# Kernel optimization log

Hardware: AMD Instinct MI355X
Metric: run time of the kernel (lower is better)

The kernel has to match this reference:

```python
import jax, jax.numpy as jnp
import numpy as np

B, NQ, NV, DIM, H, F = 32, 197, 1568, 768, 12, 8


def setup_inputs() -> dict:
    key = jax.random.key(0)
    ks = jax.random.split(key, 5)
    return {
        "x": jax.random.normal(ks[0], (B, NV, DIM), jnp.float32),
        "question": jax.random.normal(ks[1], (B, NQ, DIM), jnp.float32),
        "Wq": jax.random.normal(ks[2], (DIM, DIM), jnp.float32) * 0.02,
        "Wkv": jax.random.normal(ks[3], (DIM, 2 * DIM), jnp.float32) * 0.02,
        "Wproj": jax.random.normal(ks[4], (DIM, DIM), jnp.float32) * 0.02,
        "bproj": jnp.zeros((DIM,), jnp.float32),
        "f": F,
    }


def _heads(t, h):
    # 'b n (h d) -> (b h) n d'
    b, n, dim = t.shape
    d = dim // h
    return t.reshape(b, n, h, d).transpose(0, 2, 1, 3).reshape(b * h, n, d)


def reference(x, question, Wq, Wkv, Wproj, bproj, f):
    b, nv, dim = x.shape
    h = H
    d = dim // h
    scale = d ** -0.5

    q = _heads(question @ Wq, h) * scale          # (bh, nq, d), pre-scaled as in source
    kv = x @ Wkv
    k = _heads(kv[..., :dim], h)                  # (bh, nv, d)
    v = _heads(kv[..., dim:], h)                  # (bh, nv, d)

    cls_q, q_ = q[:, :1], q[:, 1:]                # cls token vs patch queries

    # cls token attends over ALL video tokens
    cls_sim = jnp.einsum('bid,bjd->bij', cls_q, k)
    cls_out = jnp.einsum('bij,bjd->bid', jax.nn.softmax(cls_sim, axis=-1), v)

    # patch queries attend per-frame: k,v 'b (f n) d -> (b f) n d', q_ repeat_interleave(f)
    n = nv // f
    kf = k.reshape(b * h, f, n, d)
    vf = v.reshape(b * h, f, n, d)
    sim = jnp.einsum('bqd,bfkd->bfqk', q_, kf)    # broadcast == repeat_interleave over frames
    out = jnp.einsum('bfqk,bfkd->bfqd', jax.nn.softmax(sim, axis=-1), vf)
    out = out.reshape(b * h, f * (q.shape[1] - 1), d)  # '(b f) n d -> b (f n) d'

    out = jnp.concatenate([cls_out, out], axis=1)  # (bh, 1 + f*(nq-1), d)
    n_out = out.shape[1]
    # '(b h) n d -> b n (h d)'
    out = out.reshape(b, h, n_out, d).transpose(0, 2, 1, 3).reshape(b, n_out, dim)
    return out @ Wproj + bproj
```

## Files before the change

### kernel.cpp

```cpp
#include <hip/hip_runtime.h>

typedef __bf16 bf16;
typedef __bf16 bf16x8 __attribute__((ext_vector_type(8)));
typedef __bf16 bf16x4 __attribute__((ext_vector_type(4)));
typedef __bf16 bf16x2 __attribute__((ext_vector_type(2)));
typedef float f32x4 __attribute__((ext_vector_type(4)));
typedef float f32x16 __attribute__((ext_vector_type(16)));
typedef unsigned int u32x4 __attribute__((ext_vector_type(4)));

#define MFMA16(a, b, c) __builtin_amdgcn_mfma_f32_16x16x32_bf16(a, b, c, 0, 0, 0)
#define MFMA32(a, b, c) __builtin_amdgcn_mfma_f32_32x32x16_bf16(a, b, c, 0, 0, 0)

__device__ __forceinline__ void gload_lds16(const bf16* g, bf16* l) {
  __builtin_amdgcn_global_load_lds(
      (const __attribute__((address_space(1))) void*)g,
      (__attribute__((address_space(3))) void*)l, 16, 0, 0);
}

__device__ __forceinline__ unsigned pk2(float a, float b) {
  bf16x2 t;
  t[0] = (bf16)a;
  t[1] = (bf16)b;
  return __builtin_bit_cast(unsigned, t);
}

__device__ __forceinline__ void wg_barrier() {
  __builtin_amdgcn_sched_barrier(0);
  asm volatile("s_barrier" ::: "memory");
  __builtin_amdgcn_sched_barrier(0);
}

__global__ __launch_bounds__(256) void f2b_k(const float* __restrict__ src,
                                             bf16* __restrict__ dst,
                                             long long n) {
  long long i = ((long long)blockIdx.x * 256 + threadIdx.x) * 8;
  if (i >= n) return;
  const float4 a = *(const float4*)(src + i);
  const float4 b = *(const float4*)(src + i + 4);
  bf16x8 v;
  v[0] = (bf16)a.x; v[1] = (bf16)a.y; v[2] = (bf16)a.z; v[3] = (bf16)a.w;
  v[4] = (bf16)b.x; v[5] = (bf16)b.y; v[6] = (bf16)b.z; v[7] = (bf16)b.w;
  *(bf16x8*)(dst + i) = v;
}

__global__ __launch_bounds__(256) void wconv_k(const float* __restrict__ W,
                                               bf16* __restrict__ Wt,
                                               int K, int N) {
  long long idx = (long long)blockIdx.x * 256 + threadIdx.x;
  if (idx >= (long long)K * N) return;
  int k = (int)(idx % K);
  int n = (int)(idx / K);
  Wt[idx] = (bf16)W[(long long)k * N + n];
}

__global__ __launch_bounds__(256) void pad0_k(bf16* __restrict__ Vt) {
  long long idx = (long long)blockIdx.x * 256 + threadIdx.x;
  const long long total = 3072LL * 64 * 7;
  if (idx >= total) return;
  int c = (int)(idx % 7);
  long long t = idx / 7;
  int d = (int)(t % 64);
  long long f = t / 64;
  bf16x4 z = {};
  *(bf16x4*)&Vt[(f * 64 + d) * 224 + 196 + c * 4] = z;
}

template <int MODE>
__global__ __launch_bounds__(256) void gemm_k(const bf16* __restrict__ A,
                                              const bf16* __restrict__ Bt,
                                              void* __restrict__ Cptr,
                                              const float* __restrict__ bias,
                                              int M, int N, int K) {
  __shared__ bf16 As[128 * 64];
  __shared__ bf16 Bs[128 * 64];
  const int tid = threadIdx.x;
  const int lane = tid & 63, w = tid >> 6;
  const int wm = w & 1, wn = w >> 1;
  const int col = lane & 15, quad = lane >> 4;
  const int m0 = blockIdx.x * 128, n0 = blockIdx.y * 128;

  const int rsub = lane >> 3;
  const int segg = (lane & 7) ^ rsub;
  const bf16* Ag0 = A + (long long)(m0 + w * 32 + rsub) * K + segg * 8;
  const bf16* Bg0 = Bt + (long long)(n0 + w * 32 + rsub) * K + segg * 8;
  bf16* Al0 = As + (w * 32) * 64;
  bf16* Bl0 = Bs + (w * 32) * 64;

  f32x4 acc[4][4] = {};
  const int sA = col & 7;

  for (int k0 = 0; k0 < K; k0 += 64) {
    __syncthreads();
#pragma unroll
    for (int j = 0; j < 4; ++j)
      gload_lds16(Ag0 + (long long)j * 8 * K + k0, Al0 + j * 8 * 64);
#pragma unroll
    for (int j = 0; j < 4; ++j)
      gload_lds16(Bg0 + (long long)j * 8 * K + k0, Bl0 + j * 8 * 64);
    __syncthreads();

#pragma unroll
    for (int kk2 = 0; kk2 < 2; ++kk2) {
      const int s = kk2 * 4 + quad;
      const int slot = (s ^ sA) * 8;
      bf16x8 af[4], bfr[4];
#pragma unroll
      for (int mt = 0; mt < 4; ++mt)
        af[mt] = *(const bf16x8*)&As[(wm * 64 + mt * 16 + col) * 64 + slot];
#pragma unroll
      for (int nt = 0; nt < 4; ++nt)
        bfr[nt] = *(const bf16x8*)&Bs[(wn * 64 + nt * 16 + col) * 64 + slot];
#pragma unroll
      for (int mt = 0; mt < 4; ++mt) {
#pragma unroll
        for (int nt = 0; nt < 4; ++nt)
          acc[mt][nt] = MFMA16(af[mt], bfr[nt], acc[mt][nt]);
      }
    }
  }

#pragma unroll
  for (int mt = 0; mt < 4; ++mt) {
#pragma unroll
    for (int nt = 0; nt < 4; ++nt) {
      const int gn = n0 + wn * 64 + nt * 16 + col;
#pragma unroll
      for (int r = 0; r < 4; ++r) {
        const int gm = m0 + wm * 64 + mt * 16 + quad * 4 + r;
        if (gm >= M) continue;
        const float v = acc[mt][nt][r];
        ((bf16*)Cptr)[(long long)gm * N + gn] = (bf16)(v * 0.125f);
      }
    }
  }
}

template <int MODE>
__global__ __launch_bounds__(512) void gemm256_k(
    const bf16* __restrict__ A, const bf16* __restrict__ Bt,
    void* __restrict__ Cptr, bf16* __restrict__ C2,
    const float* __restrict__ bias, int M, int N, int K,
    int NB, int qq, int rq) {
  __shared__ bf16 As[2][256 * 64];
  __shared__ bf16 Bs[2][256 * 64];
  const int tid = threadIdx.x;
  const int lane = tid & 63, w = tid >> 6;
  const int wm = w & 1, wn = w >> 1;
  const int col = lane & 15, quad = lane >> 4;

  const int bid = blockIdx.x;
  const int xcd = bid & 7, ii = bid >> 3;
  const int wg = (xcd < rq ? xcd * (qq + 1) : rq * (qq + 1) + (xcd - rq) * qq) + ii;
  const int mb = wg / NB, nb = wg - mb * NB;
  const int m0 = mb * 256, n0 = nb * 256;

  const int rsub = lane >> 3;
  const int segg = (lane & 7) ^ rsub;
  const bf16* Ag0 = A + (long long)(m0 + w * 32 + rsub) * K + segg * 8;
  const bf16* Bg0 = Bt + (long long)(n0 + w * 32 + rsub) * K + segg * 8;
  const int lbase = (w * 32) * 64;

  f32x4 acc[8][4] = {};
  const int sA = col & 7;

#pragma unroll
  for (int j = 0; j < 4; ++j) {
    gload_lds16(Ag0 + (long long)j * 8 * K, &As[0][lbase + j * 8 * 64]);
    gload_lds16(Bg0 + (long long)j * 8 * K, &Bs[0][lbase + j * 8 * 64]);
  }

  const int NT = K >> 6;
  for (int t = 0; t < NT; ++t) {
    const int cur = t & 1;
    if (t + 1 < NT) {
      const long long koff = (long long)(t + 1) * 64;
#pragma unroll
      for (int j = 0; j < 4; ++j) {
        gload_lds16(Ag0 + (long long)j * 8 * K + koff,
                    &As[cur ^ 1][lbase + j * 8 * 64]);
        gload_lds16(Bg0 + (long long)j * 8 * K + koff,
                    &Bs[cur ^ 1][lbase + j * 8 * 64]);
      }
      asm volatile("s_waitcnt vmcnt(8)");
    } else {
      asm volatile("s_waitcnt vmcnt(0)");
    }
    wg_barrier();

#pragma unroll
    for (int kk2 = 0; kk2 < 2; ++kk2) {
      const int slot = ((kk2 * 4 + quad) ^ sA) << 3;
      bf16x8 af[8], bfv[4];
#pragma unroll
      for (int mt = 0; mt < 8; ++mt)
        af[mt] = *(const bf16x8*)&As[cur][(wm * 128 + mt * 16 + col) * 64 + slot];
#pragma unroll
      for (int nt = 0; nt < 4; ++nt)
        bfv[nt] = *(const bf16x8*)&Bs[cur][(wn * 64 + nt * 16 + col) * 64 + slot];
      __builtin_amdgcn_s_setprio(1);
#pragma unroll
      for (int mt = 0; mt < 8; ++mt) {
#pragma unroll
        for (int nt = 0; nt < 4; ++nt)
          acc[mt][nt] = MFMA16(af[mt], bfv[nt], acc[mt][nt]);
      }
      __builtin_amdgcn_s_setprio(0);
    }
    wg_barrier();
  }

  if (MODE == 1) {
    bf16* Kbp = (bf16*)Cptr;
#pragma unroll
    for (int mt = 0; mt < 8; ++mt) {
      const int gm0 = m0 + wm * 128 + mt * 16 + quad * 4;
      if (gm0 >= M) continue;
      const int bb = gm0 / 1568;
      const int j0 = gm0 - bb * 1568;
      const int fr = j0 / 196;
      const int kk0 = j0 - fr * 196;
#pragma unroll
      for (int nt = 0; nt < 4; ++nt) {
        const int gn = n0 + wn * 64 + nt * 16 + col;
        if (gn < 768) {
          const int hh = gn >> 6, dd = gn & 63;
          bf16* kp = Kbp + ((long long)(bb * 12 + hh) * 1568 + j0) * 64 + dd;
#pragma unroll
          for (int r = 0; r < 4; ++r) kp[r * 64] = (bf16)acc[mt][nt][r];
        } else {
          const int g2 = gn - 768;
          const int hh = g2 >> 6, dd = g2 & 63;
          bf16x4 pv;
          pv[0] = (bf16)acc[mt][nt][0];
          pv[1] = (bf16)acc[mt][nt][1];
          pv[2] = (bf16)acc[mt][nt][2];
          pv[3] = (bf16)acc[mt][nt][3];
          *(bf16x4*)&C2[(((long long)(bb * 12 + hh) * 8 + fr) * 64 + dd) * 224 +
                        kk0] = pv;
        }
      }
    }
  } else {
#pragma unroll
    for (int mt = 0; mt < 8; ++mt) {
#pragma unroll
      for (int nt = 0; nt < 4; ++nt) {
        const int gn = n0 + wn * 64 + nt * 16 + col;
        const float bv = bias[gn];
#pragma unroll
        for (int r = 0; r < 4; ++r) {
          const int gm = m0 + wm * 128 + mt * 16 + quad * 4 + r;
          if (gm < M)
            ((float*)Cptr)[(long long)gm * N + gn] = acc[mt][nt][r] + bv;
        }
      }
    }
  }
}

__global__ __launch_bounds__(256) void attn_k(const bf16* __restrict__ qs,
                                              const bf16* __restrict__ Kb,
                                              const bf16* __restrict__ Vt,
                                              bf16* __restrict__ Ob) {
  __shared__ bf16 Ks[224 * 64];
  const int bh = blockIdx.x, fr = blockIdx.y;
  const int b = bh / 12, h = bh % 12;
  const int tid = threadIdx.x, lane = tid & 63, w = tid >> 6;
  const int col = lane & 31, half = lane >> 5;
  const bf16* Qb = qs + (long long)b * 197 * 768 + h * 64;
  const bf16* Kbase = Kb + ((long long)bh * 1568 + fr * 196) * 64;
  const bf16* Vbase = Vt + (long long)(bh * 8 + fr) * 64 * 224;

  {
    const int rsub = lane >> 3;
    const int segg = (lane & 7) ^ rsub;
    const bf16* g0 = Kbase + (long long)(w * 56 + rsub) * 64 + segg * 8;
    bf16* l0 = Ks + (w * 56) * 64;
#pragma unroll
    for (int j = 0; j < 7; ++j)
      gload_lds16(g0 + (long long)j * 8 * 64, l0 + j * 8 * 64);
  }
  __syncthreads();

  for (int mt = w; mt < 7; mt += 4) {
    const int qq = mt * 32 + col;
    const int tok = (qq < 196) ? qq + 1 : 196;
    const bf16* qp = Qb + (long long)tok * 768 + half * 8;
    bf16x8 qf[4];
#pragma unroll
    for (int t = 0; t < 4; ++t) qf[t] = *(const bf16x8*)(qp + 16 * t);

    f32x16 o0 = {}, o1 = {};
    float m = -1e30f, l = 0.f;

#pragma unroll 2
    for (int nt = 0; nt < 7; ++nt) {
      bf16x8 vf[4];
#pragma unroll
      for (int wdw = 0; wdw < 2; ++wdw)
#pragma unroll
        for (int dt = 0; dt < 2; ++dt)
          vf[wdw * 2 + dt] = *(const bf16x8*)(Vbase +
              (long long)(dt * 32 + col) * 224 + nt * 32 + wdw * 16 + half * 8);

      f32x16 s = {};
#pragma unroll
      for (int t = 0; t < 4; ++t) {
        const int row = nt * 32 + col;
        const int sgm = 2 * t + half;
        const bf16x8 kf =
            *(const bf16x8*)&Ks[row * 64 + ((sgm ^ (row & 7)) << 3)];
        s = MFMA32(kf, qf[t], s);
      }
      if (nt == 6) {
#pragma unroll
        for (int r = 0; r < 16; ++r) {
          if (r >= 4) s[r] = -1e30f;
          else if (half) s[r] = -1e30f;
        }
      }

      float tm = s[0];
#pragma unroll
      for (int r = 1; r < 16; ++r) tm = fmaxf(tm, s[r]);
      tm = fmaxf(tm, __shfl_xor(tm, 32, 64));

      if (__any(tm > m + 8.f)) {
        const float mn = fmaxf(m, tm);
        const float sc = __expf(m - mn);
        l *= sc;
#pragma unroll
        for (int r = 0; r < 16; ++r) {
          const float scr = __shfl(sc, (r & 3) + 8 * (r >> 2) + 4 * half, 64);
          o0[r] *= scr;
          o1[r] *= scr;
        }
        m = mn;
      }

      float ls = 0.f;
#pragma unroll
      for (int r = 0; r < 16; ++r) {
        s[r] = __expf(s[r] - m);
        ls += s[r];
      }
      l += ls;
      unsigned pk[8];
#pragma unroll
      for (int i = 0; i < 8; ++i) pk[i] = pk2(s[2 * i], s[2 * i + 1]);

#pragma unroll
      for (int wdw = 0; wdw < 2; ++wdw) {
        const unsigned xa = half ? pk[4 * wdw + 0] : pk[4 * wdw + 2];
        const unsigned xb = half ? pk[4 * wdw + 1] : pk[4 * wdw + 3];
        const unsigned ya = __shfl_xor(xa, 32, 64);
        const unsigned yb = __shfl_xor(xb, 32, 64);
        const unsigned oa = half ? pk[4 * wdw + 2] : pk[4 * wdw + 0];
        const unsigned ob = half ? pk[4 * wdw + 3] : pk[4 * wdw + 1];
        u32x4 wv;
        wv[0] = half ? ya : oa;
        wv[1] = half ? yb : ob;
        wv[2] = half ? oa : ya;
        wv[3] = half ? ob : yb;
        const bf16x8 pa = __builtin_bit_cast(bf16x8, wv);
        o0 = MFMA32(pa, vf[wdw * 2 + 0], o0);
        o1 = MFMA32(pa, vf[wdw * 2 + 1], o1);
      }
    }

    const float lt = l + __shfl_xor(l, 32, 64);
    const float inv = 1.f / lt;
#pragma unroll
    for (int r = 0; r < 16; ++r) {
      const int qr = (r & 3) + 8 * (r >> 2) + 4 * half;
      const float invr = __shfl(inv, qr, 64);
      const int q2 = mt * 32 + qr;
      if (q2 < 196) {
        const int token = 1 + fr * 196 + q2;
        bf16* op = Ob + ((long long)b * 1569 + token) * 768 + h * 64 + col;
        op[0] = (bf16)(o0[r] * invr);
        op[32] = (bf16)(o1[r] * invr);
      }
    }
  }
}

__global__ __launch_bounds__(256) void cls_k(const bf16* __restrict__ qs,
                                             const bf16* __restrict__ Kb,
                                             const bf16* __restrict__ Vt,
                                             bf16* __restrict__ Ob) {
  __shared__ float qsm[64];
  __shared__ float ssm[1568];
  __shared__ float red[256];
  __shared__ float osm[4][64];
  const int bh = blockIdx.x;
  const int b = bh / 12, h = bh % 12;
  const int tid = threadIdx.x;
  if (tid < 64) qsm[tid] = (float)qs[(long long)b * 197 * 768 + h * 64 + tid];
  __syncthreads();

  float lmax = -1e30f;
  for (int j = tid; j < 1568; j += 256) {
    const bf16* kp = Kb + ((long long)bh * 1568 + j) * 64;
    float s = 0.f;
#pragma unroll
    for (int seg = 0; seg < 8; ++seg) {
      const bf16x8 kv = *(const bf16x8*)(kp + seg * 8);
#pragma unroll
      for (int i = 0; i < 8; ++i) s += qsm[seg * 8 + i] * (float)kv[i];
    }
    ssm[j] = s;
    lmax = fmaxf(lmax, s);
  }
  red[tid] = lmax;
  __syncthreads();
  for (int sft = 128; sft > 0; sft >>= 1) {
    if (tid < sft) red[tid] = fmaxf(red[tid], red[tid + sft]);
    __syncthreads();
  }
  const float mx = red[0];
  __syncthreads();

  float lsum = 0.f;
  for (int j = tid; j < 1568; j += 256) {
    const float p = __expf(ssm[j] - mx);
    ssm[j] = p;
    lsum += p;
  }
  red[tid] = lsum;
  __syncthreads();
  for (int sft = 128; sft > 0; sft >>= 1) {
    if (tid < sft) red[tid] += red[tid + sft];
    __syncthreads();
  }
  const float inv = 1.f / red[0];
  __syncthreads();

  const int d = tid & 63, c = tid >> 6;
  float acc = 0.f;
  for (int fr = c * 2; fr < c * 2 + 2; ++fr) {
    const bf16* vp = Vt + ((long long)(bh * 8 + fr) * 64 + d) * 224;
    const float* pp = &ssm[fr * 196];
    for (int k = 0; k < 196; ++k) acc += pp[k] * (float)vp[k];
  }
  osm[c][d] = acc;
  __syncthreads();
  if (tid < 64) {
    const float o = (osm[0][tid] + osm[1][tid] + osm[2][tid] + osm[3][tid]) * inv;
    Ob[(long long)b * 1569 * 768 + h * 64 + tid] = (bf16)o;
  }
}

extern "C" void kernel_launch(void* const* d_in, const int* in_sizes, int n_in,
                              void* d_out, int out_size, void* d_ws, size_t ws_size,
                              hipStream_t stream) {
  const float* x        = (const float*)d_in[0];
  const float* question = (const float*)d_in[1];
  const float* Wq       = (const float*)d_in[2];
  const float* Wkv      = (const float*)d_in[3];
  const float* Wproj    = (const float*)d_in[4];
  const float* bproj    = (const float*)d_in[5];
  float* out = (float*)d_out;

  char* wsb = (char*)d_ws;
  const long long SZ_WQT  = 768LL * 768 * 2;
  const long long SZ_WKVT = 1536LL * 768 * 2;
  const long long SZ_WPT  = 768LL * 768 * 2;
  const long long SZ_QNB  = 32LL * 197 * 768 * 2;
  const long long SZ_Q    = 32LL * 197 * 768 * 2;
  const long long SZ_XO   = 50208LL * 768 * 2;
  const long long SZ_K    = 384LL * 1568 * 64 * 2;

  long long off = 0;
  bf16* Wqt  = (bf16*)(wsb + off); off += SZ_WQT;
  bf16* Wkvt = (bf16*)(wsb + off); off += SZ_WKVT;
  bf16* Wpt  = (bf16*)(wsb + off); off += SZ_WPT;
  bf16* qnb  = (bf16*)(wsb + off); off += SZ_QNB;
  bf16* qsb  = (bf16*)(wsb + off); off += SZ_Q;
  bf16* xb   = (bf16*)(wsb + off);
  bf16* Ob   = xb;
  off += SZ_XO;
  bf16* Kb   = (bf16*)(wsb + off); off += SZ_K;
  bf16* Vt   = (bf16*)(wsb + off);

  const long long nx = 32LL * 1568 * 768;
  const long long nq = 32LL * 197 * 768;
  f2b_k<<<(int)((nx / 8 + 255) / 256), 256, 0, stream>>>(x, xb, nx);
  f2b_k<<<(int)((nq / 8 + 255) / 256), 256, 0, stream>>>(question, qnb, nq);

  wconv_k<<<(768 * 768) / 256, 256, 0, stream>>>(Wq, Wqt, 768, 768);
  wconv_k<<<(768 * 1536) / 256, 256, 0, stream>>>(Wkv, Wkvt, 768, 1536);
  wconv_k<<<(768 * 768) / 256, 256, 0, stream>>>(Wproj, Wpt, 768, 768);
  pad0_k<<<(3072 * 64 * 7) / 256, 256, 0, stream>>>(Vt);

  gemm_k<0><<<dim3(50, 6), 256, 0, stream>>>(qnb, Wqt, qsb, nullptr,
                                             6304, 768, 768);
  gemm256_k<1><<<1176, 512, 0, stream>>>(xb, Wkvt, Kb, Vt, nullptr,
                                         50176, 1536, 768, 6, 147, 0);

  cls_k<<<384, 256, 0, stream>>>(qsb, Kb, Vt, Ob);
  attn_k<<<dim3(384, 8), 256, 0, stream>>>(qsb, Kb, Vt, Ob);

  gemm256_k<2><<<591, 512, 0, stream>>>(Ob, Wpt, out, nullptr, bproj,
                                        50208, 768, 768, 3, 73, 7);
}
```

Before: 823.6 us.

## Split GEMM K-step into four quadrant phases with staggered A/B prefetch

Restructures the GEMM main loop into four MFMA phases, one per 4x2 quadrant of the accumulator tile. LDS fragment reads are interleaved between the phases, and the A and B global-to-LDS prefetches are issued at different points. The aim is to overlap LDS reads and global loads with MFMA work in a ping-pong style schedule and to lower register pressure by holding fewer fragments at once. It adds more workgroup barriers per K-step and relies on sched_barrier, which could serialize execution if waves do not interleave as intended.

```diff
diff --git a/kernel.cpp b/kernel.cpp
--- a/kernel.cpp
+++ b/kernel.cpp
@@ -164,48 +164,113 @@
   const int sA = col & 7;
 
 #pragma unroll
-  for (int j = 0; j < 4; ++j) {
+  for (int j = 0; j < 4; ++j)
     gload_lds16(Ag0 + (long long)j * 8 * K, &As[0][lbase + j * 8 * 64]);
+#pragma unroll
+  for (int j = 0; j < 4; ++j)
     gload_lds16(Bg0 + (long long)j * 8 * K, &Bs[0][lbase + j * 8 * 64]);
-  }
 
   const int NT = K >> 6;
+  bf16x8 aA[4][2], bA[2][2], bB[2][2];
+
   for (int t = 0; t < NT; ++t) {
     const int cur = t & 1;
-    if (t + 1 < NT) {
-      const long long koff = (long long)(t + 1) * 64;
-#pragma unroll
-      for (int j = 0; j < 4; ++j) {
+    const bool pf = (t + 1 < NT);
+    const long long koff = (long long)(t + 1) * 64;
+
+    if (pf) {
+#pragma unroll
+      for (int j = 0; j < 4; ++j)
         gload_lds16(Ag0 + (long long)j * 8 * K + koff,
                     &As[cur ^ 1][lbase + j * 8 * 64]);
+      __builtin_amdgcn_sched_barrier(0);
+      asm volatile("s_waitcnt vmcnt(4)");
+      __builtin_amdgcn_sched_barrier(0);
+    } else {
+      __builtin_amdgcn_sched_barrier(0);
+      asm volatile("s_waitcnt vmcnt(0)");
+      __builtin_amdgcn_sched_barrier(0);
+    }
+    wg_barrier();
+#pragma unroll
+    for (int ks = 0; ks < 2; ++ks) {
+      const int slot = ((ks * 4 + quad) ^ sA) << 3;
+#pragma unroll
+      for (int mt = 0; mt < 4; ++mt)
+        aA[mt][ks] =
+            *(const bf16x8*)&As[cur][(wm * 128 + mt * 16 + col) * 64 + slot];
+#pragma unroll
+      for (int nt = 0; nt < 2; ++nt)
+        bA[nt][ks] =
+            *(const bf16x8*)&Bs[cur][(wn * 64 + nt * 16 + col) * 64 + slot];
+    }
+    __builtin_amdgcn_s_setprio(1);
+#pragma unroll
+    for (int ks = 0; ks < 2; ++ks)
+#pragma unroll
+      for (int mt = 0; mt < 4; ++mt)
+#pragma unroll
+        for (int nt = 0; nt < 2; ++nt)
+          acc[mt][nt] = MFMA16(aA[mt][ks], bA[nt][ks], acc[mt][nt]);
+    __builtin_amdgcn_s_setprio(0);
+    wg_barrier();
+
+#pragma unroll
+    for (int ks = 0; ks < 2; ++ks) {
+      const int slot = ((ks * 4 + quad) ^ sA) << 3;
+#pragma unroll
+      for (int nt = 0; nt < 2; ++nt)
+        bB[nt][ks] = *(const bf16x8*)&Bs[cur][(wn * 64 + (nt + 2) * 16 + col) *
+                                                  64 + slot];
+    }
+    if (pf) {
+#pragma unroll
+      for (int j = 0; j < 4; ++j)
         gload_lds16(Bg0 + (long long)j * 8 * K + koff,
                     &Bs[cur ^ 1][lbase + j * 8 * 64]);
-      }
-      asm volatile("s_waitcnt vmcnt(8)");
-    } else {
-      asm volatile("s_waitcnt vmcnt(0)");
-    }
-    wg_barrier();
-
-#pragma unroll
-    for (int kk2 = 0; kk2 < 2; ++kk2) {
-      const int slot = ((kk2 * 4 + quad) ^ sA) << 3;
-      bf16x8 af[8], bfv[4];
-#pragma unroll
-      for (int mt = 0; mt < 8; ++mt)
-        af[mt] = *(const bf16x8*)&As[cur][(wm * 128 + mt * 16 + col) * 64 + slot];
-#pragma unroll
-      for (int nt = 0; nt < 4; ++nt)
-        bfv[nt] = *(const bf16x8*)&Bs[cur][(wn * 64 + nt * 16 + col) * 64 + slot];
-      __builtin_amdgcn_s_setprio(1);
-#pragma unroll
-      for (int mt = 0; mt < 8; ++mt) {
-#pragma unroll
-        for (int nt = 0; nt < 4; ++nt)
-          acc[mt][nt] = MFMA16(af[mt], bfv[nt], acc[mt][nt]);
-      }
-      __builtin_amdgcn_s_setprio(0);
-    }
+    }
+    wg_barrier();
+    __builtin_amdgcn_s_setprio(1);
+#pragma unroll
+    for (int ks = 0; ks < 2; ++ks)
+#pragma unroll
+      for (int mt = 0; mt < 4; ++mt)
+#pragma unroll
+        for (int nt = 0; nt < 2; ++nt)
+          acc[mt][nt + 2] = MFMA16(aA[mt][ks], bB[nt][ks], acc[mt][nt + 2]);
+    __builtin_amdgcn_s_setprio(0);
+    wg_barrier();
+
+#pragma unroll
+    for (int ks = 0; ks < 2; ++ks) {
+      const int slot = ((ks * 4 + quad) ^ sA) << 3;
+#pragma unroll
+      for (int mt = 0; mt < 4; ++mt)
+        aA[mt][ks] = *(const bf16x8*)&As[cur][(wm * 128 + (mt + 4) * 16 + col) *
+                                                  64 + slot];
+    }
+    wg_barrier();
+    __builtin_amdgcn_s_setprio(1);
+#pragma unroll
+    for (int ks = 0; ks < 2; ++ks)
+#pragma unroll
+      for (int mt = 0; mt < 4; ++mt)
+#pragma unroll
+        for (int nt = 0; nt < 2; ++nt)
+          acc[mt + 4][nt + 2] =
+              MFMA16(aA[mt][ks], bB[nt][ks], acc[mt + 4][nt + 2]);
+    __builtin_amdgcn_s_setprio(0);
+    wg_barrier();
+
+    __builtin_amdgcn_s_setprio(1);
+#pragma unroll
+    for (int ks = 0; ks < 2; ++ks)
+#pragma unroll
+      for (int mt = 0; mt < 4; ++mt)
+#pragma unroll
+        for (int nt = 0; nt < 2; ++nt)
+          acc[mt + 4][nt] = MFMA16(aA[mt][ks], bA[nt][ks], acc[mt + 4][nt]);
+    __builtin_amdgcn_s_setprio(0);
     wg_barrier();
   }
 
```

Result: no change. 819.8 us (-0.5%).

## Make KV projection GEMM persistent with cross-tile prefetch of next job

Applied to the files above, without the earlier changes.

Replaces the 1176-block KV projection GEMM with a persistent kernel of 256 blocks. Each block loops over 4-5 output tiles, with tiles grouped by XCD (blockIdx & 7). The first K-slice of the next tile is prefetched while the last slice of the current one is computed. This removes launch and tail effects and hides the pipeline fill between tiles. The cost is a fixed schedule hardcoded to these shapes, plus the loss of the M-bound check in the epilogue.

```diff
diff --git a/kernel.cpp b/kernel.cpp
--- a/kernel.cpp
+++ b/kernel.cpp
@@ -209,12 +209,120 @@
     wg_barrier();
   }
 
-  if (MODE == 1) {
-    bf16* Kbp = (bf16*)Cptr;
+#pragma unroll
+  for (int mt = 0; mt < 8; ++mt) {
+#pragma unroll
+    for (int nt = 0; nt < 4; ++nt) {
+      const int gn = n0 + wn * 64 + nt * 16 + col;
+      const float bv = bias[gn];
+#pragma unroll
+      for (int r = 0; r < 4; ++r) {
+        const int gm = m0 + wm * 128 + mt * 16 + quad * 4 + r;
+        if (gm < M)
+          ((float*)Cptr)[(long long)gm * N + gn] = acc[mt][nt][r] + bv;
+      }
+    }
+  }
+}
+
+__global__ __launch_bounds__(512) void gemmp_k(const bf16* __restrict__ A,
+                                               const bf16* __restrict__ Bt,
+                                               bf16* __restrict__ Kb,
+                                               bf16* __restrict__ Vt) {
+  __shared__ bf16 As[2][256 * 64];
+  __shared__ bf16 Bs[2][256 * 64];
+  const int tid = threadIdx.x;
+  const int lane = tid & 63, w = tid >> 6;
+  const int wm = w & 1, wn = w >> 1;
+  const int col = lane & 15, quad = lane >> 4;
+
+  const int b = blockIdx.x;
+  const int xcd = b & 7, sub = b >> 3;
+  const int base = xcd * 147;
+  const int njobs = (sub <= 18) ? 5 : 4;
+
+  const int rsub = lane >> 3;
+  const int segg = (lane & 7) ^ rsub;
+  const int lbase = (w * 32) * 64;
+  const int sA = col & 7;
+
+  f32x4 acc[8][4] = {};
+
+  int jj = base + sub;
+  int mb = jj / 6;
+  int m0 = mb * 256, n0 = (jj - mb * 6) * 256;
+
+  {
+    const bf16* Ag = A + (long long)(m0 + w * 32 + rsub) * 768 + segg * 8;
+    const bf16* Bg = Bt + (long long)(n0 + w * 32 + rsub) * 768 + segg * 8;
+#pragma unroll
+    for (int j = 0; j < 4; ++j) {
+      gload_lds16(Ag + (long long)j * 8 * 768, &As[0][lbase + j * 8 * 64]);
+      gload_lds16(Bg + (long long)j * 8 * 768, &Bs[0][lbase + j * 8 * 64]);
+    }
+  }
+
+  int tglob = 0;
+  for (int g = 0; g < njobs; ++g) {
+    int m0n = 0, n0n = 0;
+    const bool hasNext = (g + 1 < njobs);
+    if (hasNext) {
+      const int j2 = base + sub + 32 * (g + 1);
+      const int mb2 = j2 / 6;
+      m0n = mb2 * 256;
+      n0n = (j2 - mb2 * 6) * 256;
+    }
+
+    for (int kt = 0; kt < 12; ++kt, ++tglob) {
+      const int cur = tglob & 1;
+      if (kt < 11 || hasNext) {
+        const int sm0 = (kt < 11) ? m0 : m0n;
+        const int sn0 = (kt < 11) ? n0 : n0n;
+        const int skt = (kt < 11) ? kt + 1 : 0;
+        const bf16* Ag =
+            A + (long long)(sm0 + w * 32 + rsub) * 768 + skt * 64 + segg * 8;
+        const bf16* Bg =
+            Bt + (long long)(sn0 + w * 32 + rsub) * 768 + skt * 64 + segg * 8;
+#pragma unroll
+        for (int j = 0; j < 4; ++j) {
+          gload_lds16(Ag + (long long)j * 8 * 768,
+                      &As[cur ^ 1][lbase + j * 8 * 64]);
+          gload_lds16(Bg + (long long)j * 8 * 768,
+                      &Bs[cur ^ 1][lbase + j * 8 * 64]);
+        }
+        asm volatile("s_waitcnt vmcnt(8)");
+      } else {
+        asm volatile("s_waitcnt vmcnt(0)");
+      }
+      wg_barrier();
+
+#pragma unroll
+      for (int kk2 = 0; kk2 < 2; ++kk2) {
+        const int slot = ((kk2 * 4 + quad) ^ sA) << 3;
+        bf16x8 af[8], bfv[4];
+#pragma unroll
+        for (int mt = 0; mt < 8; ++mt)
+          af[mt] =
+              *(const bf16x8*)&As[cur][(wm * 128 + mt * 16 + col) * 64 + slot];
+#pragma unroll
+        for (int nt = 0; nt < 4; ++nt)
+          bfv[nt] =
+              *(const bf16x8*)&Bs[cur][(wn * 64 + nt * 16 + col) * 64 + slot];
+        __builtin_amdgcn_s_setprio(1);
+#pragma unroll
+        for (int mt = 0; mt < 8; ++mt) {
+#pragma unroll
+          for (int nt = 0; nt < 4; ++nt)
+            acc[mt][nt] = MFMA16(af[mt], bfv[nt], acc[mt][nt]);
+        }
+        __builtin_amdgcn_s_setprio(0);
+      }
+      wg_barrier();
+    }
+
 #pragma unroll
     for (int mt = 0; mt < 8; ++mt) {
       const int gm0 = m0 + wm * 128 + mt * 16 + quad * 4;
-      if (gm0 >= M) continue;
       const int bb = gm0 / 1568;
       const int j0 = gm0 - bb * 1568;
       const int fr = j0 / 196;
@@ -224,7 +332,7 @@
         const int gn = n0 + wn * 64 + nt * 16 + col;
         if (gn < 768) {
           const int hh = gn >> 6, dd = gn & 63;
-          bf16* kp = Kbp + ((long long)(bb * 12 + hh) * 1568 + j0) * 64 + dd;
+          bf16* kp = Kb + ((long long)(bb * 12 + hh) * 1568 + j0) * 64 + dd;
 #pragma unroll
           for (int r = 0; r < 4; ++r) kp[r * 64] = (bf16)acc[mt][nt][r];
         } else {
@@ -235,26 +343,17 @@
           pv[1] = (bf16)acc[mt][nt][1];
           pv[2] = (bf16)acc[mt][nt][2];
           pv[3] = (bf16)acc[mt][nt][3];
-          *(bf16x4*)&C2[(((long long)(bb * 12 + hh) * 8 + fr) * 64 + dd) * 224 +
+          *(bf16x4*)&Vt[(((long long)(bb * 12 + hh) * 8 + fr) * 64 + dd) * 224 +
                         kk0] = pv;
         }
       }
     }
-  } else {
-#pragma unroll
-    for (int mt = 0; mt < 8; ++mt) {
-#pragma unroll
-      for (int nt = 0; nt < 4; ++nt) {
-        const int gn = n0 + wn * 64 + nt * 16 + col;
-        const float bv = bias[gn];
-#pragma unroll
-        for (int r = 0; r < 4; ++r) {
-          const int gm = m0 + wm * 128 + mt * 16 + quad * 4 + r;
-          if (gm < M)
-            ((float*)Cptr)[(long long)gm * N + gn] = acc[mt][nt][r] + bv;
-        }
-      }
-    }
+#pragma unroll
+    for (int mt = 0; mt < 8; ++mt)
+#pragma unroll
+      for (int nt = 0; nt < 4; ++nt) acc[mt][nt] = (f32x4){0.f, 0.f, 0.f, 0.f};
+    m0 = m0n;
+    n0 = n0n;
   }
 }
 
@@ -495,8 +594,7 @@
 
   gemm_k<0><<<dim3(50, 6), 256, 0, stream>>>(qnb, Wqt, qsb, nullptr,
                                              6304, 768, 768);
-  gemm256_k<1><<<1176, 512, 0, stream>>>(xb, Wkvt, Kb, Vt, nullptr,
-                                         50176, 1536, 768, 6, 147, 0);
+  gemmp_k<<<256, 512, 0, stream>>>(xb, Wkvt, Kb, Vt);
 
   cls_k<<<384, 256, 0, stream>>>(qsb, Kb, Vt, Ob);
   attn_k<<<dim3(384, 8), 256, 0, stream>>>(qsb, Kb, Vt, Ob);
```

Result: no change. 823.0 us (-0.1%).
